# Performance work log

Measured on AMD Instinct MI355X. Metric: run time of the kernel, lower is better.

Reference implementation:

```python
import jax, jax.numpy as jnp
import numpy as np

N_EMBD = 1024
H_DIM = 1024
NB = 16          # blocks resolved by _find_dynamic_num_blocks for all projections
N_MEM = 128
N_FORG = H_DIM - N_MEM
RANK = 64
LOG_DT_INIT = -2.0
EPS = 1.1920929e-07  # torch fp32 finfo eps used by F.rms_norm


def rms_norm(x):
    return x * jax.lax.rsqrt(jnp.mean(jnp.square(x), axis=-1, keepdims=True) + EPS)


def silu(x):
    return x * jax.nn.sigmoid(x)


def blockdiag(x, w):
    # x: [..., nb*bi], w: [nb, bo, bi] -> [..., nb*bo]
    nb, bo, bi = w.shape
    xs = x.reshape(*x.shape[:-1], nb, bi)
    y = jnp.einsum('...ni,noi->...no', xs, w)
    return y.reshape(*x.shape[:-1], nb * bo)


def causal_scan(drive, a):
    # drive: [B,T,D] float32, a: [D] per-channel decay; causal conv with kernel a^t via FFT
    B, T, D = drive.shape
    steps = jnp.arange(T, dtype=jnp.float32)
    kernel = jnp.exp(jnp.log(jnp.maximum(a, 1e-6))[:, None] * steps[None, :])  # [D,T]
    n_fft = 1 << int(2 * T - 1).bit_length()
    df = jnp.fft.rfft(drive.astype(jnp.float32).transpose(0, 2, 1), n=n_fft, axis=-1)
    kf = jnp.fft.rfft(kernel, n=n_fft, axis=-1)
    y = jnp.fft.irfft(df * kf[None], n=n_fft, axis=-1)[..., :T]
    return y.transpose(0, 2, 1).astype(drive.dtype)


def geom_gain(a, K):
    one_minus = 1.0 - a
    safe = jnp.maximum(one_minus, 1e-8)
    return jnp.where(jnp.abs(one_minus) < 1e-6,
                     jnp.full_like(a, float(K)),
                     (1.0 - a ** K) / safe)


def setup_inputs() -> dict:
    key = jax.random.key(0)
    ks = jax.random.split(key, 10)
    s = 0.02
    bi_e, bo_h = N_EMBD // NB, H_DIM // NB
    bi_p = (2 * N_EMBD + H_DIM) // NB
    bo_e = N_EMBD // NB
    return {
        'x': jax.random.normal(ks[0], (4, 4096, N_EMBD), dtype=jnp.float32),
        'active_k': 4,
        'b_seq_w': jax.random.normal(ks[1], (NB, bo_h, bi_e), jnp.float32) * s,
        'b_depth_w': jax.random.normal(ks[2], (NB, bo_h, bi_e), jnp.float32) * s,
        'w_post_w': jax.random.normal(ks[3], (NB, bo_h, bi_p), jnp.float32) * s,
        'w_local_w': jax.random.normal(ks[4], (NB, bo_e, H_DIM // NB), jnp.float32) * s,
        'lr_A': jax.random.normal(ks[5], (N_EMBD, RANK), jnp.float32) * s,
        'lr_B': jax.random.normal(ks[6], (RANK, H_DIM), jnp.float32) * s,
        'log_A_seq': jnp.zeros((H_DIM,), jnp.float32),
        'log_dt_seq': jnp.full((H_DIM,), LOG_DT_INIT, jnp.float32),
        'log_A_depth': jnp.zeros((N_FORG,), jnp.float32),
        'log_dt_depth': jnp.full((N_FORG,), LOG_DT_INIT, jnp.float32),
    }


def reference(x, active_k, b_seq_w, b_depth_w, w_post_w, w_local_w, lr_A, lr_B,
              log_A_seq, log_dt_seq, log_A_depth, log_dt_depth):
    K = int(active_k)
    e = rms_norm(x)
    shifted_e = jnp.pad(e[:, :-1], ((0, 0), (1, 0), (0, 0)))
    a_seq = jnp.exp(-jnp.exp(log_A_seq) * jnp.exp(log_dt_seq))
    h_seq = causal_scan(silu(blockdiag(e, b_seq_w)), a_seq)
    a_forg = jnp.exp(-jnp.exp(log_A_depth) * jnp.exp(log_dt_depth))
    a_depth = jnp.concatenate([jnp.ones((N_MEM,), a_forg.dtype), a_forg], axis=0)
    gain = geom_gain(a_depth, K).astype(x.dtype)
    h_depth = gain * silu(blockdiag(e, b_depth_w))
    h = h_seq + h_depth
    r = silu(blockdiag(jnp.concatenate([rms_norm(h), e, shifted_e], axis=-1), w_post_w))
    out = x + blockdiag(r, w_local_w) + (r @ lr_B.T) @ lr_A.T
    return out
```

## Files before the change

kernel.cpp:

```cpp
#include <hip/hip_runtime.h>

#define B_ 4
#define T_ 4096
#define D_ 1024
#define R_ (B_*T_)
#define CHUNK_ 64
#define NCH_ (T_/CHUNK_)
#define EPS_ 1.1920929e-07f
#define P_ ((size_t)R_*64)

typedef unsigned short ushort_t;
typedef __attribute__((ext_vector_type(8))) short short8;
typedef __attribute__((ext_vector_type(4))) float f32x4;

__device__ __forceinline__ float silu_f(float v){ return v / (1.0f + __expf(-v)); }

__device__ __forceinline__ ushort_t f2bf(float f){
    unsigned u = __float_as_uint(f);
    unsigned r = u + 0x7fffu + ((u>>16)&1u);
    return (ushort_t)(r>>16);
}
__device__ __forceinline__ float bf2f(ushort_t s){ return __uint_as_float(((unsigned)s)<<16); }

__device__ __forceinline__ f32x4 mfma16(short8 a, short8 b, f32x4 c){
    return __builtin_amdgcn_mfma_f32_16x16x32_bf16(a, b, c, 0, 0, 0);
}


__global__ void prep_k(const float* __restrict__ s0, const float* __restrict__ s1,
                       const float* __restrict__ s2, const float* __restrict__ s3,
                       const float* __restrict__ s4, const float* __restrict__ s5,
                       ushort_t* __restrict__ d0, ushort_t* __restrict__ d1,
                       ushort_t* __restrict__ d2, ushort_t* __restrict__ d3,
                       ushort_t* __restrict__ d4, ushort_t* __restrict__ d5,
                       const float* __restrict__ logA_seq, const float* __restrict__ logdt_seq,
                       const float* __restrict__ logA_dep, const float* __restrict__ logdt_dep,
                       const int* __restrict__ active_k,
                       float* __restrict__ aseq, float* __restrict__ apowC, float* __restrict__ gain){
    int i = blockIdx.x*256 + threadIdx.x;
    if      (i < 65536)   d0[i] = f2bf(s0[i]);
    else if (i < 131072)  d1[i-65536] = f2bf(s1[i-65536]);
    else if (i < 327680)  d2[i-131072] = f2bf(s2[i-131072]);
    else if (i < 393216)  d3[i-327680] = f2bf(s3[i-327680]);
    else if (i < 458752)  d4[i-393216] = f2bf(s4[i-393216]);
    else if (i < 524288)  d5[i-458752] = f2bf(s5[i-458752]);
    else if (i < 524288 + D_){
        int d = i - 524288;
        float K = (float)(*active_k);
        float a = expf(-expf(logA_seq[d]) * expf(logdt_seq[d]));
        a = fmaxf(a, 1e-6f);
        aseq[d] = a;
        apowC[d] = powf(a, (float)CHUNK_);
        float g;
        if (d < 128) {
            g = K;
        } else {
            float ad = expf(-expf(logA_dep[d-128]) * expf(logdt_dep[d-128]));
            float om = 1.0f - ad;
            if (fabsf(om) < 1e-6f) g = K;
            else g = (1.0f - powf(ad, K)) / fmaxf(om, 1e-8f);
        }
        gain[d] = g;
    }
}

__global__ __launch_bounds__(256) void rmsbf_k(const float* __restrict__ x, ushort_t* __restrict__ e){
    int row = blockIdx.x;
    int tid = threadIdx.x;
    float4 v = ((const float4*)(x + (size_t)row*D_))[tid];
    float ss = v.x*v.x + v.y*v.y + v.z*v.z + v.w*v.w;
    for (int off=32; off; off>>=1) ss += __shfl_down(ss, off, 64);
    __shared__ float red[4];
    if ((tid&63)==0) red[tid>>6] = ss;
    __syncthreads();
    float tot = red[0]+red[1]+red[2]+red[3];
    float scale = 1.0f / sqrtf(tot*(1.0f/D_) + EPS_);
    ushort4 o;
    o.x = f2bf(v.x*scale); o.y = f2bf(v.y*scale); o.z = f2bf(v.z*scale); o.w = f2bf(v.w*scale);
    int col = tid*4;
    *(ushort4*)(e + (size_t)(col>>6)*P_ + (size_t)row*64 + (col&63)) = o;
}

__global__ __launch_bounds__(256) void bd2s_k(const ushort_t* __restrict__ e,
        const ushort_t* __restrict__ wseq, const ushort_t* __restrict__ wdep,
        const float* __restrict__ gain, const float* __restrict__ aseq,
        ushort_t* __restrict__ hsum, float* __restrict__ carry){
    __shared__ __align__(16) ushort_t sd[4][16][72];
    __shared__ __align__(16) ushort_t sh[4][16][72];
    int wave = threadIdx.x>>6, lane = threadIdx.x&63;
    int m = lane&15, quad = lane>>4;
    int orow = lane>>2, oq = lane&3;
    int n = blockIdx.y;
    int chunk0 = blockIdx.x*256 + wave*64;

    short8 bs[2][4], bd[2][4];
    #pragma unroll
    for (int s=0;s<2;++s)
        #pragma unroll
        for (int c=0;c<4;++c){
            bs[s][c] = *(const short8*)(wseq + n*4096 + (c*16+m)*64 + s*32 + quad*8);
            bd[s][c] = *(const short8*)(wdep + n*4096 + (c*16+m)*64 + s*32 + quad*8);
        }
    float g[4];
    #pragma unroll
    for (int c=0;c<4;++c) g[c] = gain[n*64 + c*16 + m];

    float a = aseq[n*64 + lane];
    float hh = 0.f;

    #pragma unroll
    for (int t=0;t<4;++t){
        int r0 = chunk0 + t*16;
        const ushort_t* ab = e + (size_t)n*P_ + (size_t)(r0+m)*64 + quad*8;
        short8 a0 = *(const short8*)ab;
        short8 a1 = *(const short8*)(ab + 32);
        f32x4 accs[4], accd[4];
        #pragma unroll
        for (int c=0;c<4;++c){
            accs[c]=(f32x4)0.f; accd[c]=(f32x4)0.f;
            accs[c]=mfma16(a0, bs[0][c], accs[c]);
            accd[c]=mfma16(a0, bd[0][c], accd[c]);
            accs[c]=mfma16(a1, bs[1][c], accs[c]);
            accd[c]=mfma16(a1, bd[1][c], accd[c]);
        }
        #pragma unroll
        for (int c=0;c<4;++c)
            #pragma unroll
            for (int r=0;r<4;++r){
                sd[wave][quad*4+r][c*16+m] = f2bf(silu_f(accs[c][r]));
                sh[wave][quad*4+r][c*16+m] = f2bf(g[c]*silu_f(accd[c][r]));
            }
        #pragma unroll
        for (int s=0;s<16;++s){
            hh = fmaf(a, hh, bf2f(sd[wave][s][lane]));
            sd[wave][s][lane] = f2bf(hh + bf2f(sh[wave][s][lane]));
        }
        ushort_t* db = hsum + (size_t)n*P_ + (size_t)(r0+orow)*64;
        #pragma unroll
        for (int it=0;it<2;++it)
            *(short8*)(db + (it*4+oq)*8) = *(const short8*)&sd[wave][orow][(it*4+oq)*8];
    }
    carry[(size_t)(chunk0>>6)*D_ + n*64 + lane] = hh;
}

__global__ __launch_bounds__(256) void scan2_k(float* __restrict__ carry, const float* __restrict__ apowC){
    int tid = blockIdx.x*256 + threadIdx.x;
    int d = tid & (D_-1);
    int b = tid >> 10;
    float aC = apowC[d];
    float pref = 0.f;
    for (int c=0;c<NCH_;++c){
        size_t idx = (size_t)(b*NCH_+c)*D_ + d;
        float s = carry[idx];
        carry[idx] = pref;
        pref = fmaf(aC, pref, s);
    }
}

__global__ __launch_bounds__(256) void scan3_k(const ushort_t* __restrict__ hsum,
                                               const float* __restrict__ aseq,
                                               const float* __restrict__ carry,
                                               ushort_t* __restrict__ h){
    int tid = blockIdx.x*256 + threadIdx.x;
    int d0g  = (tid&7)*8;
    int trip = tid>>3;
    int n  = trip & 15;
    int bc = trip >> 4;
    int b  = bc >> 6;
    int c  = bc & (NCH_-1);
    int d  = n*64 + d0g;
    float a[8], P[8], apow[8];
    #pragma unroll
    for (int j=0;j<8;++j){
        a[j] = aseq[d+j];
        P[j] = carry[(size_t)bc*D_ + d + j];
        apow[j] = a[j];
    }
    size_t base = (size_t)n*P_ + (size_t)(b*T_ + c*CHUNK_)*64 + d0g;
    for (int s=0; s<CHUNK_; ++s){
        short8 v = *(const short8*)(hsum + base + (size_t)s*64);
        short8 o;
        #pragma unroll
        for (int j=0;j<8;++j){
            o[j] = (short)f2bf(bf2f((ushort_t)v[j]) + P[j]*apow[j]);
            apow[j] *= a[j];
        }
        *(short8*)(h + base + (size_t)s*64) = o;
    }
}

__global__ __launch_bounds__(256) void scale_k(const ushort_t* __restrict__ h, float* __restrict__ scale){
    int wave = threadIdx.x>>6, lane = threadIdx.x&63;
    int row = blockIdx.x*4 + wave;
    int pl = lane>>2, q = lane&3;
    const ushort_t* hb = h + (size_t)pl*P_ + (size_t)row*64 + q*16;
    short8 v0 = *(const short8*)hb;
    short8 v1 = *(const short8*)(hb + 8);
    float ss = 0.f;
    #pragma unroll
    for (int j=0;j<8;++j){ float f0 = bf2f((ushort_t)v0[j]); float f1 = bf2f((ushort_t)v1[j]); ss += f0*f0 + f1*f1; }
    for (int off=32; off; off>>=1) ss += __shfl_down(ss, off, 64);
    if (lane==0) scale[row] = rsqrtf(ss*(1.0f/D_) + EPS_);
}

__global__ __launch_bounds__(256) void post_k(const ushort_t* __restrict__ h,
                                              const float* __restrict__ scale,
                                              const ushort_t* __restrict__ e,
                                              const ushort_t* __restrict__ wpost, ushort_t* __restrict__ rout){
    __shared__ __align__(16) ushort_t st[4][16][72];
    int wave = threadIdx.x>>6, lane = threadIdx.x&63;
    int m = lane&15, quad = lane>>4;
    int orow = lane>>2, oq = lane&3;
    int n = blockIdx.y;
    int row0 = blockIdx.x*128 + wave*32 + m;

    float scl[2];
    #pragma unroll
    for (int t=0;t<2;++t) scl[t] = (n*192 < 1024) ? scale[row0 + t*16] : 0.f;

    f32x4 acc[2][4];
    #pragma unroll
    for (int t=0;t<2;++t)
        #pragma unroll
        for (int c=0;c<4;++c) acc[t][c]=(f32x4)0.f;

    #pragma unroll 1
    for (int s=0;s<6;++s){
        int g0 = n*192 + s*32;
        short8 bw[4];
        #pragma unroll
        for (int c=0;c<4;++c)
            bw[c] = *(const short8*)(wpost + n*(64*192) + (c*16+m)*192 + s*32 + quad*8);
        #pragma unroll
        for (int t=0;t<2;++t){
            int row = row0 + t*16;
            short8 af;
            if (g0 < 1024){
                short8 hv = *(const short8*)(h + (size_t)(g0>>6)*P_ + (size_t)row*64 + (g0&63) + quad*8);
                float sc = scl[t];
                #pragma unroll
                for (int j=0;j<8;++j) af[j] = (short)f2bf(bf2f((ushort_t)hv[j])*sc);
            } else if (g0 < 2048){
                int ge = g0 - 1024;
                af = *(const short8*)(e + (size_t)(ge>>6)*P_ + (size_t)row*64 + (ge&63) + quad*8);
            } else {
                int ge = g0 - 2048;
                if ((row & (T_-1)) == 0) af = short8{0,0,0,0,0,0,0,0};
                else af = *(const short8*)(e + (size_t)(ge>>6)*P_ + (size_t)(row-1)*64 + (ge&63) + quad*8);
            }
            #pragma unroll
            for (int c=0;c<4;++c)
                acc[t][c] = mfma16(af, bw[c], acc[t][c]);
        }
    }
    #pragma unroll
    for (int t=0;t<2;++t){
        int r0 = blockIdx.x*128 + wave*32 + t*16;
        #pragma unroll
        for (int c=0;c<4;++c)
            #pragma unroll
            for (int r=0;r<4;++r)
                st[wave][quad*4+r][c*16+m] = f2bf(silu_f(acc[t][c][r]));
        ushort_t* db = rout + (size_t)n*P_ + (size_t)(r0+orow)*64;
        #pragma unroll
        for (int it=0;it<2;++it)
            *(short8*)(db + (it*4+oq)*8) = *(const short8*)&st[wave][orow][(it*4+oq)*8];
    }
}

__global__ __launch_bounds__(256) void rlow_k(const ushort_t* __restrict__ r, const ushort_t* __restrict__ lrB,
                                              ushort_t* __restrict__ rlow){
    __shared__ __align__(16) float sacc[4][16][68];
    int wave = threadIdx.x>>6, lane = threadIdx.x&63;
    int m = lane&15, quad = lane>>4;
    int r0 = blockIdx.x*16;
    f32x4 acc[4];
    #pragma unroll
    for (int c=0;c<4;++c) acc[c]=(f32x4)0.f;
    #pragma unroll
    for (int s=0;s<8;++s){
        int col = wave*256 + s*32;
        short8 a = *(const short8*)(r + (size_t)(col>>6)*P_ + (size_t)(r0+m)*64 + (col&63) + quad*8);
        #pragma unroll
        for (int c=0;c<4;++c){
            short8 b = *(const short8*)(lrB + (c*16+m)*1024 + col + quad*8);
            acc[c] = mfma16(a, b, acc[c]);
        }
    }
    #pragma unroll
    for (int c=0;c<4;++c)
        #pragma unroll
        for (int r2=0;r2<4;++r2)
            sacc[wave][quad*4+r2][c*16+m] = acc[c][r2];
    __syncthreads();
    int row  = threadIdx.x>>4;
    int col4 = (threadIdx.x&15)*4;
    float4 v0 = *(const float4*)&sacc[0][row][col4];
    float4 v1 = *(const float4*)&sacc[1][row][col4];
    float4 v2 = *(const float4*)&sacc[2][row][col4];
    float4 v3 = *(const float4*)&sacc[3][row][col4];
    ushort4 o;
    o.x = f2bf(v0.x+v1.x+v2.x+v3.x);
    o.y = f2bf(v0.y+v1.y+v2.y+v3.y);
    o.z = f2bf(v0.z+v1.z+v2.z+v3.z);
    o.w = f2bf(v0.w+v1.w+v2.w+v3.w);
    *(ushort4*)(rlow + (size_t)(r0+row)*64 + col4) = o;
}

__global__ __launch_bounds__(256) void out_k(const float* __restrict__ x, const ushort_t* __restrict__ r,
        const ushort_t* __restrict__ rlow, const ushort_t* __restrict__ wloc, const ushort_t* __restrict__ lrA,
        float* __restrict__ out){
    __shared__ __align__(16) float st[4][16][68];
    int wave = threadIdx.x>>6, lane = threadIdx.x&63;
    int m = lane&15, quad = lane>>4;
    int orow = lane>>2, oq = lane&3;
    int n = blockIdx.y;

    short8 wl[2][4], la[4][2];
    #pragma unroll
    for (int c=0;c<4;++c)
        #pragma unroll
        for (int s=0;s<2;++s){
            wl[s][c] = *(const short8*)(wloc + n*4096 + (c*16+m)*64 + s*32 + quad*8);
            la[c][s] = *(const short8*)(lrA + (size_t)(n*64 + c*16 + m)*64 + s*32 + quad*8);
        }
    #pragma unroll
    for (int t=0;t<2;++t){
        int r0 = blockIdx.x*128 + wave*32 + t*16;
        const float* xb = x + (size_t)(r0+orow)*D_ + n*64;
        float4 xv[4];
        #pragma unroll
        for (int it=0;it<4;++it) xv[it] = *(const float4*)(xb + (it*4+oq)*4);

        const ushort_t* lb = rlow + (size_t)(r0+m)*64 + quad*8;
        short8 al0 = *(const short8*)lb;
        short8 al1 = *(const short8*)(lb + 32);
        const ushort_t* ab = r + (size_t)n*P_ + (size_t)(r0+m)*64 + quad*8;
        short8 ar0 = *(const short8*)ab;
        short8 ar1 = *(const short8*)(ab + 32);
        f32x4 acc[4];
        #pragma unroll
        for (int c=0;c<4;++c){
            acc[c]=(f32x4)0.f;
            acc[c]=mfma16(al0, la[c][0], acc[c]);
            acc[c]=mfma16(al1, la[c][1], acc[c]);
            acc[c]=mfma16(ar0, wl[0][c], acc[c]);
            acc[c]=mfma16(ar1, wl[1][c], acc[c]);
        }
        #pragma unroll
        for (int c=0;c<4;++c)
            #pragma unroll
            for (int r2=0;r2<4;++r2)
                st[wave][quad*4+r2][c*16+m] = acc[c][r2];
        float* ob = out + (size_t)(r0+orow)*D_ + n*64;
        #pragma unroll
        for (int it=0;it<4;++it){
            float4 v = *(const float4*)&st[wave][orow][(it*4+oq)*4];
            v.x += xv[it].x; v.y += xv[it].y; v.z += xv[it].z; v.w += xv[it].w;
            *(float4*)(ob + (it*4+oq)*4) = v;
        }
    }
}

extern "C" void kernel_launch(void* const* d_in, const int* in_sizes, int n_in,
                              void* d_out, int out_size, void* d_ws, size_t ws_size,
                              hipStream_t stream) {
    const float* x         = (const float*)d_in[0];
    const int*   active_k  = (const int*)  d_in[1];
    const float* b_seq_w   = (const float*)d_in[2];
    const float* b_depth_w = (const float*)d_in[3];
    const float* w_post_w  = (const float*)d_in[4];
    const float* w_local_w = (const float*)d_in[5];
    const float* lr_A      = (const float*)d_in[6];
    const float* lr_B      = (const float*)d_in[7];
    const float* logA_seq  = (const float*)d_in[8];
    const float* logdt_seq = (const float*)d_in[9];
    const float* logA_dep  = (const float*)d_in[10];
    const float* logdt_dep = (const float*)d_in[11];

    float* ws    = (float*)d_ws;
    float* carry = ws;
    float* aseq  = carry + (size_t)B_*NCH_*D_;
    float* apowC = aseq + D_;
    float* gain  = apowC + D_;
    float* scale = gain + D_;
    ushort_t* ub       = (ushort_t*)(scale + R_);
    ushort_t* e_bf     = ub;
    ushort_t* hsum_bf  = e_bf + (size_t)R_*D_;
    ushort_t* h_bf     = hsum_bf + (size_t)R_*D_;
    ushort_t* r_bf     = h_bf + (size_t)R_*D_;
    ushort_t* rlow_bf  = r_bf + (size_t)R_*D_;
    ushort_t* wseq_bf  = rlow_bf + (size_t)R_*64;
    ushort_t* wdep_bf  = wseq_bf + 65536;
    ushort_t* wpost_bf = wdep_bf + 65536;
    ushort_t* wloc_bf  = wpost_bf + 196608;
    ushort_t* lrA_bf   = wloc_bf + 65536;
    ushort_t* lrB_bf   = lrA_bf + 65536;

    prep_k<<<(524288 + D_ + 255)/256, 256, 0, stream>>>(
        b_seq_w, b_depth_w, w_post_w, w_local_w, lr_A, lr_B,
        wseq_bf, wdep_bf, wpost_bf, wloc_bf, lrA_bf, lrB_bf,
        logA_seq, logdt_seq, logA_dep, logdt_dep, active_k, aseq, apowC, gain);

    rmsbf_k<<<R_, 256, 0, stream>>>(x, e_bf);
    bd2s_k <<<dim3(R_/256, 16), 256, 0, stream>>>(e_bf, wseq_bf, wdep_bf, gain, aseq,
                                                  hsum_bf, carry);
    scan2_k<<<(B_*D_)/256, 256, 0, stream>>>(carry, apowC);
    scan3_k<<<(B_*NCH_*D_/8)/256, 256, 0, stream>>>(hsum_bf, aseq, carry, h_bf);
    scale_k<<<R_/4, 256, 0, stream>>>(h_bf, scale);
    post_k <<<dim3(R_/128, 16), 256, 0, stream>>>(h_bf, scale, e_bf, wpost_bf, r_bf);
    rlow_k <<<R_/16, 256, 0, stream>>>(r_bf, lrB_bf, rlow_bf);
    out_k  <<<dim3(R_/128, 16), 256, 0, stream>>>(x, r_bf, rlow_bf, wloc_bf, lrA_bf, (float*)d_out);
}
```

Baseline: 292.6 us.

## Fuse scan carry-fixup into scale and post kernels via precomputed decay-power table

Removes the scan3 kernel, which read hsum and wrote a full bf16 h tensor. Instead, scale_k and post_k each apply the carry correction h = hsum + carry*a^s on the fly, using a per-channel power table precomputed in prep_k. This saves one full read and one full write of an R×D bf16 tensor, at the cost of recomputing the correction twice and extra fp32 loads of carry and the table. post_k also changes from 32 to 16 rows per wave and gathers all A fragments before the MFMA loop.

```diff
diff --git a/kernel.cpp b/kernel.cpp
--- a/kernel.cpp
+++ b/kernel.cpp
@@ -36,7 +36,8 @@
                        const float* __restrict__ logA_seq, const float* __restrict__ logdt_seq,
                        const float* __restrict__ logA_dep, const float* __restrict__ logdt_dep,
                        const int* __restrict__ active_k,
-                       float* __restrict__ aseq, float* __restrict__ apowC, float* __restrict__ gain){
+                       float* __restrict__ aseq, float* __restrict__ apowC,
+                       float* __restrict__ gain, float* __restrict__ apowtab){
     int i = blockIdx.x*256 + threadIdx.x;
     if      (i < 65536)   d0[i] = f2bf(s0[i]);
     else if (i < 131072)  d1[i-65536] = f2bf(s1[i-65536]);
@@ -51,6 +52,8 @@
         a = fmaxf(a, 1e-6f);
         aseq[d] = a;
         apowC[d] = powf(a, (float)CHUNK_);
+        float ap = a;
+        for (int s2=0;s2<CHUNK_;++s2){ apowtab[s2*D_ + d] = ap; ap *= a; }
         float g;
         if (d < 128) {
             g = K;
@@ -157,53 +160,34 @@
     }
 }
 
-__global__ __launch_bounds__(256) void scan3_k(const ushort_t* __restrict__ hsum,
-                                               const float* __restrict__ aseq,
+__global__ __launch_bounds__(256) void scale_k(const ushort_t* __restrict__ hsum,
                                                const float* __restrict__ carry,
-                                               ushort_t* __restrict__ h){
-    int tid = blockIdx.x*256 + threadIdx.x;
-    int d0g  = (tid&7)*8;
-    int trip = tid>>3;
-    int n  = trip & 15;
-    int bc = trip >> 4;
-    int b  = bc >> 6;
-    int c  = bc & (NCH_-1);
-    int d  = n*64 + d0g;
-    float a[8], P[8], apow[8];
-    #pragma unroll
-    for (int j=0;j<8;++j){
-        a[j] = aseq[d+j];
-        P[j] = carry[(size_t)bc*D_ + d + j];
-        apow[j] = a[j];
-    }
-    size_t base = (size_t)n*P_ + (size_t)(b*T_ + c*CHUNK_)*64 + d0g;
-    for (int s=0; s<CHUNK_; ++s){
-        short8 v = *(const short8*)(hsum + base + (size_t)s*64);
-        short8 o;
-        #pragma unroll
-        for (int j=0;j<8;++j){
-            o[j] = (short)f2bf(bf2f((ushort_t)v[j]) + P[j]*apow[j]);
-            apow[j] *= a[j];
-        }
-        *(short8*)(h + base + (size_t)s*64) = o;
-    }
-}
-
-__global__ __launch_bounds__(256) void scale_k(const ushort_t* __restrict__ h, float* __restrict__ scale){
+                                               const float* __restrict__ apowtab,
+                                               float* __restrict__ scale){
     int wave = threadIdx.x>>6, lane = threadIdx.x&63;
     int row = blockIdx.x*4 + wave;
+    int bc = row>>6, srow = row&63;
     int pl = lane>>2, q = lane&3;
-    const ushort_t* hb = h + (size_t)pl*P_ + (size_t)row*64 + q*16;
+    int d0 = pl*64 + q*16;
+    const ushort_t* hb = hsum + (size_t)pl*P_ + (size_t)row*64 + q*16;
     short8 v0 = *(const short8*)hb;
     short8 v1 = *(const short8*)(hb + 8);
+    const float* cp = carry + (size_t)bc*D_ + d0;
+    const float* ap = apowtab + (size_t)srow*D_ + d0;
     float ss = 0.f;
     #pragma unroll
-    for (int j=0;j<8;++j){ float f0 = bf2f((ushort_t)v0[j]); float f1 = bf2f((ushort_t)v1[j]); ss += f0*f0 + f1*f1; }
+    for (int j=0;j<8;++j){
+        float f0 = bf2f((ushort_t)v0[j]) + cp[j]*ap[j];
+        float f1 = bf2f((ushort_t)v1[j]) + cp[j+8]*ap[j+8];
+        ss += f0*f0 + f1*f1;
+    }
     for (int off=32; off; off>>=1) ss += __shfl_down(ss, off, 64);
     if (lane==0) scale[row] = rsqrtf(ss*(1.0f/D_) + EPS_);
 }
 
-__global__ __launch_bounds__(256) void post_k(const ushort_t* __restrict__ h,
+__global__ __launch_bounds__(256) void post_k(const ushort_t* __restrict__ hsum,
+                                              const float* __restrict__ carry,
+                                              const float* __restrict__ apowtab,
                                               const float* __restrict__ scale,
                                               const ushort_t* __restrict__ e,
                                               const ushort_t* __restrict__ wpost, ushort_t* __restrict__ rout){
@@ -212,60 +196,57 @@
     int m = lane&15, quad = lane>>4;
     int orow = lane>>2, oq = lane&3;
     int n = blockIdx.y;
-    int row0 = blockIdx.x*128 + wave*32 + m;
-
-    float scl[2];
-    #pragma unroll
-    for (int t=0;t<2;++t) scl[t] = (n*192 < 1024) ? scale[row0 + t*16] : 0.f;
-
-    f32x4 acc[2][4];
-    #pragma unroll
-    for (int t=0;t<2;++t)
-        #pragma unroll
-        for (int c=0;c<4;++c) acc[t][c]=(f32x4)0.f;
-
-    #pragma unroll 1
+    int row = blockIdx.x*64 + wave*16 + m;
+    int bc = row>>6, srow = row&63;
+
+    float sc = (n*192 < 1024) ? scale[row] : 0.f;
+
+    short8 af[6];
+    #pragma unroll
     for (int s=0;s<6;++s){
         int g0 = n*192 + s*32;
+        if (g0 < 1024){
+            int d0 = g0 + quad*8;
+            short8 hv = *(const short8*)(hsum + (size_t)(g0>>6)*P_ + (size_t)row*64 + (g0&63) + quad*8);
+            const float* cp = carry + (size_t)bc*D_ + d0;
+            const float* ap = apowtab + (size_t)srow*D_ + d0;
+            #pragma unroll
+            for (int j=0;j<8;++j){
+                float hf = bf2f((ushort_t)hv[j]) + cp[j]*ap[j];
+                af[s][j] = (short)f2bf(hf*sc);
+            }
+        } else if (g0 < 2048){
+            int ge = g0 - 1024;
+            af[s] = *(const short8*)(e + (size_t)(ge>>6)*P_ + (size_t)row*64 + (ge&63) + quad*8);
+        } else {
+            int ge = g0 - 2048;
+            if ((row & (T_-1)) == 0) af[s] = short8{0,0,0,0,0,0,0,0};
+            else af[s] = *(const short8*)(e + (size_t)(ge>>6)*P_ + (size_t)(row-1)*64 + (ge&63) + quad*8);
+        }
+    }
+
+    f32x4 acc[4];
+    #pragma unroll
+    for (int c=0;c<4;++c) acc[c]=(f32x4)0.f;
+    #pragma unroll
+    for (int s=0;s<6;++s){
         short8 bw[4];
         #pragma unroll
         for (int c=0;c<4;++c)
             bw[c] = *(const short8*)(wpost + n*(64*192) + (c*16+m)*192 + s*32 + quad*8);
         #pragma unroll
-        for (int t=0;t<2;++t){
-            int row = row0 + t*16;
-            short8 af;
-            if (g0 < 1024){
-                short8 hv = *(const short8*)(h + (size_t)(g0>>6)*P_ + (size_t)row*64 + (g0&63) + quad*8);
-                float sc = scl[t];
-                #pragma unroll
-                for (int j=0;j<8;++j) af[j] = (short)f2bf(bf2f((ushort_t)hv[j])*sc);
-            } else if (g0 < 2048){
-                int ge = g0 - 1024;
-                af = *(const short8*)(e + (size_t)(ge>>6)*P_ + (size_t)row*64 + (ge&63) + quad*8);
-            } else {
-                int ge = g0 - 2048;
-                if ((row & (T_-1)) == 0) af = short8{0,0,0,0,0,0,0,0};
-                else af = *(const short8*)(e + (size_t)(ge>>6)*P_ + (size_t)(row-1)*64 + (ge&63) + quad*8);
-            }
-            #pragma unroll
-            for (int c=0;c<4;++c)
-                acc[t][c] = mfma16(af, bw[c], acc[t][c]);
-        }
-    }
-    #pragma unroll
-    for (int t=0;t<2;++t){
-        int r0 = blockIdx.x*128 + wave*32 + t*16;
-        #pragma unroll
         for (int c=0;c<4;++c)
-            #pragma unroll
-            for (int r=0;r<4;++r)
-                st[wave][quad*4+r][c*16+m] = f2bf(silu_f(acc[t][c][r]));
-        ushort_t* db = rout + (size_t)n*P_ + (size_t)(r0+orow)*64;
-        #pragma unroll
-        for (int it=0;it<2;++it)
-            *(short8*)(db + (it*4+oq)*8) = *(const short8*)&st[wave][orow][(it*4+oq)*8];
-    }
+            acc[c] = mfma16(af[s], bw[c], acc[c]);
+    }
+    #pragma unroll
+    for (int c=0;c<4;++c)
+        #pragma unroll
+        for (int r=0;r<4;++r)
+            st[wave][quad*4+r][c*16+m] = f2bf(silu_f(acc[c][r]));
+    ushort_t* db = rout + (size_t)n*P_ + (size_t)(blockIdx.x*64 + wave*16 + orow)*64;
+    #pragma unroll
+    for (int it=0;it<2;++it)
+        *(short8*)(db + (it*4+oq)*8) = *(const short8*)&st[wave][orow][(it*4+oq)*8];
 }
 
 __global__ __launch_bounds__(256) void rlow_k(const ushort_t* __restrict__ r, const ushort_t* __restrict__ lrB,
@@ -378,17 +359,17 @@
     const float* logA_dep  = (const float*)d_in[10];
     const float* logdt_dep = (const float*)d_in[11];
 
-    float* ws    = (float*)d_ws;
-    float* carry = ws;
-    float* aseq  = carry + (size_t)B_*NCH_*D_;
-    float* apowC = aseq + D_;
-    float* gain  = apowC + D_;
-    float* scale = gain + D_;
-    ushort_t* ub       = (ushort_t*)(scale + R_);
+    float* ws      = (float*)d_ws;
+    float* carry   = ws;
+    float* aseq    = carry + (size_t)B_*NCH_*D_;
+    float* apowC   = aseq + D_;
+    float* gain    = apowC + D_;
+    float* scale   = gain + D_;
+    float* apowtab = scale + R_;
+    ushort_t* ub       = (ushort_t*)(apowtab + (size_t)CHUNK_*D_);
     ushort_t* e_bf     = ub;
     ushort_t* hsum_bf  = e_bf + (size_t)R_*D_;
-    ushort_t* h_bf     = hsum_bf + (size_t)R_*D_;
-    ushort_t* r_bf     = h_bf + (size_t)R_*D_;
+    ushort_t* r_bf     = hsum_bf + (size_t)R_*D_;
     ushort_t* rlow_bf  = r_bf + (size_t)R_*D_;
     ushort_t* wseq_bf  = rlow_bf + (size_t)R_*64;
     ushort_t* wdep_bf  = wseq_bf + 65536;
@@ -400,15 +381,14 @@
     prep_k<<<(524288 + D_ + 255)/256, 256, 0, stream>>>(
         b_seq_w, b_depth_w, w_post_w, w_local_w, lr_A, lr_B,
         wseq_bf, wdep_bf, wpost_bf, wloc_bf, lrA_bf, lrB_bf,
-        logA_seq, logdt_seq, logA_dep, logdt_dep, active_k, aseq, apowC, gain);
+        logA_seq, logdt_seq, logA_dep, logdt_dep, active_k, aseq, apowC, gain, apowtab);
 
     rmsbf_k<<<R_, 256, 0, stream>>>(x, e_bf);
     bd2s_k <<<dim3(R_/256, 16), 256, 0, stream>>>(e_bf, wseq_bf, wdep_bf, gain, aseq,
                                                   hsum_bf, carry);
     scan2_k<<<(B_*D_)/256, 256, 0, stream>>>(carry, apowC);
-    scan3_k<<<(B_*NCH_*D_/8)/256, 256, 0, stream>>>(hsum_bf, aseq, carry, h_bf);
-    scale_k<<<R_/4, 256, 0, stream>>>(h_bf, scale);
-    post_k <<<dim3(R_/128, 16), 256, 0, stream>>>(h_bf, scale, e_bf, wpost_bf, r_bf);
+    scale_k<<<R_/4, 256, 0, stream>>>(hsum_bf, carry, apowtab, scale);
+    post_k <<<dim3(R_/64, 16), 256, 0, stream>>>(hsum_bf, carry, apowtab, scale, e_bf, wpost_bf, r_bf);
     rlow_k <<<R_/16, 256, 0, stream>>>(r_bf, lrB_bf, rlow_bf);
     out_k  <<<dim3(R_/128, 16), 256, 0, stream>>>(x, r_bf, rlow_bf, wloc_bf, lrA_bf, (float*)d_out);
 }
```

Result: slower. 300.5 us (+2.7%).

## Fuse post projection, low-rank reduction and output kernels into one

Applied to the files above, without the earlier changes.

Three kernels (post blockdiag+silu, r@lrB, and the output blockdiag plus low-rank update) are merged into one kernel per 16-row tile. The intermediate r stays in LDS instead of going to global memory, and the rlow buffer and two launches are removed. The cost is a 16-row tile with each wave covering 4 blocks, so weights are reloaded per 16 rows rather than per 128. LDS use also grows to about 40KB per workgroup, which may lower occupancy.

```diff
diff --git a/kernel.cpp b/kernel.cpp
--- a/kernel.cpp
+++ b/kernel.cpp
@@ -203,41 +203,33 @@
     if (lane==0) scale[row] = rsqrtf(ss*(1.0f/D_) + EPS_);
 }
 
-__global__ __launch_bounds__(256) void post_k(const ushort_t* __restrict__ h,
-                                              const float* __restrict__ scale,
-                                              const ushort_t* __restrict__ e,
-                                              const ushort_t* __restrict__ wpost, ushort_t* __restrict__ rout){
-    __shared__ __align__(16) ushort_t st[4][16][72];
+__global__ __launch_bounds__(256) void por_k(const float* __restrict__ x,
+        const ushort_t* __restrict__ h, const float* __restrict__ scale,
+        const ushort_t* __restrict__ e, const ushort_t* __restrict__ wpost,
+        const ushort_t* __restrict__ lrB, const ushort_t* __restrict__ wloc,
+        const ushort_t* __restrict__ lrA, float* __restrict__ out){
+    __shared__ __align__(16) ushort_t r_lds[16][1032];
+    __shared__ __align__(16) float sacc[4][16][68];
+    __shared__ __align__(16) ushort_t rl_lds[16][72];
     int wave = threadIdx.x>>6, lane = threadIdx.x&63;
     int m = lane&15, quad = lane>>4;
     int orow = lane>>2, oq = lane&3;
-    int n = blockIdx.y;
-    int row0 = blockIdx.x*128 + wave*32 + m;
-
-    float scl[2];
-    #pragma unroll
-    for (int t=0;t<2;++t) scl[t] = (n*192 < 1024) ? scale[row0 + t*16] : 0.f;
-
-    f32x4 acc[2][4];
-    #pragma unroll
-    for (int t=0;t<2;++t)
-        #pragma unroll
-        for (int c=0;c<4;++c) acc[t][c]=(f32x4)0.f;
-
-    #pragma unroll 1
-    for (int s=0;s<6;++s){
-        int g0 = n*192 + s*32;
-        short8 bw[4];
-        #pragma unroll
-        for (int c=0;c<4;++c)
-            bw[c] = *(const short8*)(wpost + n*(64*192) + (c*16+m)*192 + s*32 + quad*8);
-        #pragma unroll
-        for (int t=0;t<2;++t){
-            int row = row0 + t*16;
+    int r0 = blockIdx.x*16;
+    int row = r0 + m;
+
+    #pragma unroll
+    for (int nn=0; nn<4; ++nn){
+        int n = wave*4 + nn;
+        float sc = (n < 6) ? scale[row] : 0.f;
+        f32x4 acc[4];
+        #pragma unroll
+        for (int c=0;c<4;++c) acc[c]=(f32x4)0.f;
+        #pragma unroll
+        for (int s=0;s<6;++s){
+            int g0 = n*192 + s*32;
             short8 af;
             if (g0 < 1024){
                 short8 hv = *(const short8*)(h + (size_t)(g0>>6)*P_ + (size_t)row*64 + (g0&63) + quad*8);
-                float sc = scl[t];
                 #pragma unroll
                 for (int j=0;j<8;++j) af[j] = (short)f2bf(bf2f((ushort_t)hv[j])*sc);
             } else if (g0 < 2048){
@@ -249,95 +241,74 @@
                 else af = *(const short8*)(e + (size_t)(ge>>6)*P_ + (size_t)(row-1)*64 + (ge&63) + quad*8);
             }
             #pragma unroll
-            for (int c=0;c<4;++c)
-                acc[t][c] = mfma16(af, bw[c], acc[t][c]);
-        }
-    }
-    #pragma unroll
-    for (int t=0;t<2;++t){
-        int r0 = blockIdx.x*128 + wave*32 + t*16;
-        #pragma unroll
-        for (int c=0;c<4;++c)
-            #pragma unroll
-            for (int r=0;r<4;++r)
-                st[wave][quad*4+r][c*16+m] = f2bf(silu_f(acc[t][c][r]));
-        ushort_t* db = rout + (size_t)n*P_ + (size_t)(r0+orow)*64;
-        #pragma unroll
-        for (int it=0;it<2;++it)
-            *(short8*)(db + (it*4+oq)*8) = *(const short8*)&st[wave][orow][(it*4+oq)*8];
-    }
-}
-
-__global__ __launch_bounds__(256) void rlow_k(const ushort_t* __restrict__ r, const ushort_t* __restrict__ lrB,
-                                              ushort_t* __restrict__ rlow){
-    __shared__ __align__(16) float sacc[4][16][68];
-    int wave = threadIdx.x>>6, lane = threadIdx.x&63;
-    int m = lane&15, quad = lane>>4;
-    int r0 = blockIdx.x*16;
-    f32x4 acc[4];
-    #pragma unroll
-    for (int c=0;c<4;++c) acc[c]=(f32x4)0.f;
-    #pragma unroll
-    for (int s=0;s<8;++s){
-        int col = wave*256 + s*32;
-        short8 a = *(const short8*)(r + (size_t)(col>>6)*P_ + (size_t)(r0+m)*64 + (col&63) + quad*8);
-        #pragma unroll
-        for (int c=0;c<4;++c){
-            short8 b = *(const short8*)(lrB + (c*16+m)*1024 + col + quad*8);
-            acc[c] = mfma16(a, b, acc[c]);
-        }
-    }
-    #pragma unroll
-    for (int c=0;c<4;++c)
-        #pragma unroll
-        for (int r2=0;r2<4;++r2)
-            sacc[wave][quad*4+r2][c*16+m] = acc[c][r2];
+            for (int c=0;c<4;++c){
+                short8 bw = *(const short8*)(wpost + n*(64*192) + (c*16+m)*192 + s*32 + quad*8);
+                acc[c] = mfma16(af, bw, acc[c]);
+            }
+        }
+        #pragma unroll
+        for (int c=0;c<4;++c)
+            #pragma unroll
+            for (int rr=0;rr<4;++rr)
+                r_lds[quad*4+rr][n*64 + c*16 + m] = f2bf(silu_f(acc[c][rr]));
+    }
     __syncthreads();
-    int row  = threadIdx.x>>4;
-    int col4 = (threadIdx.x&15)*4;
-    float4 v0 = *(const float4*)&sacc[0][row][col4];
-    float4 v1 = *(const float4*)&sacc[1][row][col4];
-    float4 v2 = *(const float4*)&sacc[2][row][col4];
-    float4 v3 = *(const float4*)&sacc[3][row][col4];
-    ushort4 o;
-    o.x = f2bf(v0.x+v1.x+v2.x+v3.x);
-    o.y = f2bf(v0.y+v1.y+v2.y+v3.y);
-    o.z = f2bf(v0.z+v1.z+v2.z+v3.z);
-    o.w = f2bf(v0.w+v1.w+v2.w+v3.w);
-    *(ushort4*)(rlow + (size_t)(r0+row)*64 + col4) = o;
-}
-
-__global__ __launch_bounds__(256) void out_k(const float* __restrict__ x, const ushort_t* __restrict__ r,
-        const ushort_t* __restrict__ rlow, const ushort_t* __restrict__ wloc, const ushort_t* __restrict__ lrA,
-        float* __restrict__ out){
-    __shared__ __align__(16) float st[4][16][68];
-    int wave = threadIdx.x>>6, lane = threadIdx.x&63;
-    int m = lane&15, quad = lane>>4;
-    int orow = lane>>2, oq = lane&3;
-    int n = blockIdx.y;
-
-    short8 wl[2][4], la[4][2];
-    #pragma unroll
-    for (int c=0;c<4;++c)
-        #pragma unroll
-        for (int s=0;s<2;++s){
-            wl[s][c] = *(const short8*)(wloc + n*4096 + (c*16+m)*64 + s*32 + quad*8);
-            la[c][s] = *(const short8*)(lrA + (size_t)(n*64 + c*16 + m)*64 + s*32 + quad*8);
-        }
-    #pragma unroll
-    for (int t=0;t<2;++t){
-        int r0 = blockIdx.x*128 + wave*32 + t*16;
+
+    {
+        f32x4 racc[4];
+        #pragma unroll
+        for (int c=0;c<4;++c) racc[c]=(f32x4)0.f;
+        #pragma unroll
+        for (int s=0;s<8;++s){
+            int col = wave*256 + s*32;
+            short8 a = *(const short8*)&r_lds[m][col + quad*8];
+            #pragma unroll
+            for (int c=0;c<4;++c){
+                short8 b = *(const short8*)(lrB + (c*16+m)*1024 + col + quad*8);
+                racc[c] = mfma16(a, b, racc[c]);
+            }
+        }
+        #pragma unroll
+        for (int c=0;c<4;++c)
+            #pragma unroll
+            for (int rr=0;rr<4;++rr)
+                sacc[wave][quad*4+rr][c*16+m] = racc[c][rr];
+    }
+    __syncthreads();
+    {
+        int rrow = threadIdx.x>>4;
+        int col4 = (threadIdx.x&15)*4;
+        float4 v0 = *(const float4*)&sacc[0][rrow][col4];
+        float4 v1 = *(const float4*)&sacc[1][rrow][col4];
+        float4 v2 = *(const float4*)&sacc[2][rrow][col4];
+        float4 v3 = *(const float4*)&sacc[3][rrow][col4];
+        rl_lds[rrow][col4+0] = f2bf(v0.x+v1.x+v2.x+v3.x);
+        rl_lds[rrow][col4+1] = f2bf(v0.y+v1.y+v2.y+v3.y);
+        rl_lds[rrow][col4+2] = f2bf(v0.z+v1.z+v2.z+v3.z);
+        rl_lds[rrow][col4+3] = f2bf(v0.w+v1.w+v2.w+v3.w);
+    }
+    __syncthreads();
+
+    short8 al0 = *(const short8*)&rl_lds[m][quad*8];
+    short8 al1 = *(const short8*)&rl_lds[m][32 + quad*8];
+    #pragma unroll
+    for (int nn=0; nn<4; ++nn){
+        int n = wave*4 + nn;
+        short8 wl[2][4], la[4][2];
+        #pragma unroll
+        for (int c=0;c<4;++c)
+            #pragma unroll
+            for (int s=0;s<2;++s){
+                wl[s][c] = *(const short8*)(wloc + n*4096 + (c*16+m)*64 + s*32 + quad*8);
+                la[c][s] = *(const short8*)(lrA + (size_t)(n*64 + c*16 + m)*64 + s*32 + quad*8);
+            }
         const float* xb = x + (size_t)(r0+orow)*D_ + n*64;
         float4 xv[4];
         #pragma unroll
         for (int it=0;it<4;++it) xv[it] = *(const float4*)(xb + (it*4+oq)*4);
 
-        const ushort_t* lb = rlow + (size_t)(r0+m)*64 + quad*8;
-        short8 al0 = *(const short8*)lb;
-        short8 al1 = *(const short8*)(lb + 32);
-        const ushort_t* ab = r + (size_t)n*P_ + (size_t)(r0+m)*64 + quad*8;
-        short8 ar0 = *(const short8*)ab;
-        short8 ar1 = *(const short8*)(ab + 32);
+        short8 ar0 = *(const short8*)&r_lds[m][n*64 + quad*8];
+        short8 ar1 = *(const short8*)&r_lds[m][n*64 + 32 + quad*8];
         f32x4 acc[4];
         #pragma unroll
         for (int c=0;c<4;++c){
@@ -350,12 +321,12 @@
         #pragma unroll
         for (int c=0;c<4;++c)
             #pragma unroll
-            for (int r2=0;r2<4;++r2)
-                st[wave][quad*4+r2][c*16+m] = acc[c][r2];
+            for (int rr=0;rr<4;++rr)
+                sacc[wave][quad*4+rr][c*16+m] = acc[c][rr];
         float* ob = out + (size_t)(r0+orow)*D_ + n*64;
         #pragma unroll
         for (int it=0;it<4;++it){
-            float4 v = *(const float4*)&st[wave][orow][(it*4+oq)*4];
+            float4 v = *(const float4*)&sacc[wave][orow][(it*4+oq)*4];
             v.x += xv[it].x; v.y += xv[it].y; v.z += xv[it].z; v.w += xv[it].w;
             *(float4*)(ob + (it*4+oq)*4) = v;
         }
@@ -388,9 +359,7 @@
     ushort_t* e_bf     = ub;
     ushort_t* hsum_bf  = e_bf + (size_t)R_*D_;
     ushort_t* h_bf     = hsum_bf + (size_t)R_*D_;
-    ushort_t* r_bf     = h_bf + (size_t)R_*D_;
-    ushort_t* rlow_bf  = r_bf + (size_t)R_*D_;
-    ushort_t* wseq_bf  = rlow_bf + (size_t)R_*64;
+    ushort_t* wseq_bf  = h_bf + (size_t)R_*D_;
     ushort_t* wdep_bf  = wseq_bf + 65536;
     ushort_t* wpost_bf = wdep_bf + 65536;
     ushort_t* wloc_bf  = wpost_bf + 196608;
@@ -408,7 +377,6 @@
     scan2_k<<<(B_*D_)/256, 256, 0, stream>>>(carry, apowC);
     scan3_k<<<(B_*NCH_*D_/8)/256, 256, 0, stream>>>(hsum_bf, aseq, carry, h_bf);
     scale_k<<<R_/4, 256, 0, stream>>>(h_bf, scale);
-    post_k <<<dim3(R_/128, 16), 256, 0, stream>>>(h_bf, scale, e_bf, wpost_bf, r_bf);
-    rlow_k <<<R_/16, 256, 0, stream>>>(r_bf, lrB_bf, rlow_bf);
-    out_k  <<<dim3(R_/128, 16), 256, 0, stream>>>(x, r_bf, rlow_bf, wloc_bf, lrA_bf, (float*)d_out);
-}
+    por_k  <<<R_/16, 256, 0, stream>>>(x, h_bf, scale, e_bf, wpost_bf, lrB_bf, wloc_bf, lrA_bf,
+                                       (float*)d_out);
+}
```

After: 321.0 us. 9.7% more time.
